# Kernel optimization log

Measured on AMD Instinct MI355X. Metric: run time of the kernel, lower is better.

The kernel has to match this reference:

```python
import jax, jax.numpy as jnp
import numpy as np

D_MODEL = 1024
N_HEADS = 16
D_HEAD = D_MODEL // N_HEADS


def setup_inputs() -> dict:
    key = jax.random.key(0)
    ks = jax.random.split(key, 5)
    B, T = 2, 2048
    x = jax.random.normal(ks[0], (B, T, D_MODEL), dtype=jnp.float32)
    s = 1.0 / np.sqrt(D_MODEL)
    W_qkv = jax.random.normal(ks[1], (D_MODEL, 3 * D_MODEL), dtype=jnp.float32) * s
    b_qkv = jnp.zeros((3 * D_MODEL,), dtype=jnp.float32)
    W_proj = jax.random.normal(ks[2], (D_MODEL, D_MODEL), dtype=jnp.float32) * s
    b_proj = jnp.zeros((D_MODEL,), dtype=jnp.float32)
    return {"x": x, "W_qkv": W_qkv, "b_qkv": b_qkv, "W_proj": W_proj, "b_proj": b_proj}


def reference(x, W_qkv, b_qkv, W_proj, b_proj):
    B, T, C = x.shape
    qkv = x @ W_qkv + b_qkv                      # [B,T,3C]
    q, k, v = jnp.split(qkv, 3, axis=-1)
    # [B,T,C] -> [B,H,T,Dh]
    def to_heads(t):
        return t.reshape(B, T, N_HEADS, D_HEAD).transpose(0, 2, 1, 3)
    q, k, v = to_heads(q), to_heads(k), to_heads(v)
    scale = 1.0 / np.sqrt(D_HEAD).astype(np.float32)
    scores = jnp.einsum('bhqd,bhkd->bhqk', q, k) * scale  # [B,H,T,T]
    causal = jnp.tril(jnp.ones((T, T), dtype=bool))
    scores = jnp.where(causal, scores, -jnp.inf)
    attn = jax.nn.softmax(scores, axis=-1)
    out = jnp.einsum('bhqk,bhkd->bhqd', attn, v)          # [B,H,T,Dh]
    out = out.transpose(0, 2, 1, 3).reshape(B, T, C)
    return out @ W_proj + b_proj
```

## Files before the change

### kernel.cpp

```cpp
#include <hip/hip_runtime.h>
#include <hip/hip_bf16.h>
#include <cstdint>


using u16 = unsigned short;
using u32 = unsigned int;

typedef __bf16 bf16x8 __attribute__((ext_vector_type(8)));
typedef float f32x4 __attribute__((ext_vector_type(4)));

#define AS1 __attribute__((address_space(1)))
#define AS3 __attribute__((address_space(3)))

__device__ __forceinline__ u16 f2bf(float f) {
  u32 u = __float_as_uint(f);
  u += 0x7fffu + ((u >> 16) & 1u);
  return (u16)(u >> 16);
}
__device__ __forceinline__ u32 pack2bf(float a, float b) {
  u32 ua = __float_as_uint(a) + 0x8000u;
  u32 ub = __float_as_uint(b) + 0x8000u;
  return (ua >> 16) | (ub & 0xffff0000u);
}

__global__ __launch_bounds__(256) void prep(const float* __restrict__ x,
                                            u16* __restrict__ xb,
                                            const float* __restrict__ W0,
                                            u16* __restrict__ T0,
                                            const float* __restrict__ W1,
                                            u16* __restrict__ T1) {
  const int bx = blockIdx.x;
  const int tid = threadIdx.x;
  if (bx < 4096) {
    const int i = bx * 256 + tid;
    float4 v = ((const float4*)x)[i];
    ushort4 o;
    o.x = f2bf(v.x); o.y = f2bf(v.y); o.z = f2bf(v.z); o.w = f2bf(v.w);
    ((ushort4*)xb)[i] = o;
    return;
  }
  __shared__ float t[32][33];
  const int idx = bx - 4096;
  const int bxx = idx & 127, by = idx >> 7;
  const float* W; u16* Wt; int N, n0;
  if (bxx < 96) { W = W0; Wt = T0; N = 3072; n0 = bxx * 32; }
  else          { W = W1; Wt = T1; N = 1024; n0 = (bxx - 96) * 32; }
  const int k0 = by * 32;
  const int tx = tid & 31, ty = tid >> 5;
#pragma unroll
  for (int i = 0; i < 4; ++i)
    t[ty + i * 8][tx] = W[(size_t)(k0 + ty + i * 8) * N + n0 + tx];
  __syncthreads();
#pragma unroll
  for (int i = 0; i < 4; ++i)
    Wt[(size_t)(n0 + ty + i * 8) * 1024 + k0 + tx] = f2bf(t[tx][ty + i * 8]);
}

__global__ __launch_bounds__(256) void gemm_qkv(const u16* __restrict__ A,
                                                const u16* __restrict__ Bt,
                                                const float* __restrict__ bias,
                                                u16* __restrict__ qb,
                                                u16* __restrict__ KF,
                                                u16* __restrict__ VF,
                                                float sc_val) {
  constexpr int BM = 128, BK = 32;
  constexpr int K = 1024;
  __shared__ __align__(16) u16 lA[BM * BK];
  __shared__ __align__(16) u16 lB[BM * BK];
  const int tid  = threadIdx.x;
  const int lane = tid & 63;
  const int wave = tid >> 6;
  const int bm = blockIdx.x * BM;
  const int bn = blockIdx.y * BM;
  const int wr = (wave >> 1) * 64;
  const int wc = (wave & 1) * 64;

  f32x4 acc[4][4] = {};

  const int f0 = (wave << 10) + (lane << 4);
  const int f1 = f0 + 4096;
  const int r0 = f0 >> 6, c0 = (f0 & 63) >> 1;
  const int r1 = f1 >> 6, c1 = (f1 & 63) >> 1;

  const int arow = wr + (lane & 15);
  const int brow = wc + (lane & 15);
  const int kk   = (lane >> 4) << 3;

  for (int k0 = 0; k0 < K; k0 += BK) {
    __builtin_amdgcn_global_load_lds((AS1 const void*)(A + (size_t)(bm + r0) * K + k0 + c0),
                                     (AS3 void*)(lA + (wave << 9)), 16, 0, 0);
    __builtin_amdgcn_global_load_lds((AS1 const void*)(A + (size_t)(bm + r1) * K + k0 + c1),
                                     (AS3 void*)(lA + ((wave + 4) << 9)), 16, 0, 0);
    __builtin_amdgcn_global_load_lds((AS1 const void*)(Bt + (size_t)(bn + r0) * K + k0 + c0),
                                     (AS3 void*)(lB + (wave << 9)), 16, 0, 0);
    __builtin_amdgcn_global_load_lds((AS1 const void*)(Bt + (size_t)(bn + r1) * K + k0 + c1),
                                     (AS3 void*)(lB + ((wave + 4) << 9)), 16, 0, 0);
    __syncthreads();

    bf16x8 af[4], bfr[4];
#pragma unroll
    for (int mi = 0; mi < 4; ++mi)
      af[mi] = *(const bf16x8*)&lA[(arow + mi * 16) * BK + kk];
#pragma unroll
    for (int ni = 0; ni < 4; ++ni)
      bfr[ni] = *(const bf16x8*)&lB[(brow + ni * 16) * BK + kk];
#pragma unroll
    for (int mi = 0; mi < 4; ++mi)
#pragma unroll
      for (int ni = 0; ni < 4; ++ni)
        acc[mi][ni] = __builtin_amdgcn_mfma_f32_16x16x32_bf16(af[mi], bfr[ni],
                                                              acc[mi][ni], 0, 0, 0);
    __syncthreads();
  }

  const int crow0 = bm + wr + ((lane >> 4) << 2);
  const int ccol0 = bn + wc + (lane & 15);
  if (bn < 1024) {
#pragma unroll
    for (int ni = 0; ni < 4; ++ni) {
      const int n = ccol0 + ni * 16;
      const float bv = bias[n];
#pragma unroll
      for (int mi = 0; mi < 4; ++mi) {
        const int m0 = crow0 + mi * 16;
#pragma unroll
        for (int r = 0; r < 4; ++r)
          qb[(size_t)(m0 + r) * 1024 + n] = f2bf((acc[mi][ni][r] + bv) * sc_val);
      }
    }
  } else if (bn < 2048) {
#pragma unroll
    for (int ni = 0; ni < 4; ++ni) {
      const int n  = ccol0 + ni * 16;
      const int hk = (n - 1024) >> 6;
      const int d  = (n - 1024) & 63;
      const int hh = d >> 5, qd = (d >> 3) & 3, j = d & 7;
      const float bv = bias[n];
#pragma unroll
      for (int mi = 0; mi < 4; ++mi) {
#pragma unroll
        for (int r = 0; r < 4; ++r) {
          const int t  = crow0 + mi * 16 + r;
          const int bb = t >> 11, tt = t & 2047;
          const int kt = tt >> 6, mm = (tt >> 4) & 3, l = tt & 15;
          KF[((size_t)((bb * 16 + hk) * 32 + kt) * 8 + mm * 2 + hh) * 512 +
             (qd * 16 + l) * 8 + j] = f2bf(acc[mi][ni][r] + bv);
        }
      }
    }
  } else {
#pragma unroll
    for (int ni = 0; ni < 4; ++ni) {
      const int n  = ccol0 + ni * 16;
      const int hv = (n - 2048) >> 6;
      const int d  = (n - 2048) & 63;
      const int di = d >> 4, l = d & 15;
      const float bv = bias[n];
#pragma unroll
      for (int mi = 0; mi < 4; ++mi) {
#pragma unroll
        for (int r = 0; r < 4; ++r) {
          const int t  = crow0 + mi * 16 + r;
          const int bb = t >> 11, tt = t & 2047;
          const int kt = tt >> 6, to = tt & 63;
          const int mq = to >> 4, qd2 = (to >> 2) & 3, rr = to & 3;
          const int hh = mq >> 1, j = (mq & 1) * 4 + rr;
          VF[((size_t)((bb * 16 + hv) * 32 + kt) * 8 + hh * 4 + di) * 512 +
             (qd2 * 16 + l) * 8 + j] = f2bf(acc[mi][ni][r] + bv);
        }
      }
    }
  }
}

__global__ __launch_bounds__(256) void gemm_proj(const u16* __restrict__ A,
                                                 const u16* __restrict__ Bt,
                                                 const float* __restrict__ bias,
                                                 float* __restrict__ C) {
  constexpr int BM = 128, BN = 64, BK = 32;
  constexpr int K = 1024, N = 1024;
  __shared__ __align__(16) u16 lA[BM * BK];
  __shared__ __align__(16) u16 lB[BN * BK];
  const int tid  = threadIdx.x;
  const int lane = tid & 63;
  const int wave = tid >> 6;
  const int bm = blockIdx.x * BM;
  const int bn = blockIdx.y * BN;
  const int wr = wave * 32;

  f32x4 acc[2][4] = {};

  const int f0 = (wave << 10) + (lane << 4);
  const int f1 = f0 + 4096;
  const int ar0 = f0 >> 6, ac0 = (f0 & 63) >> 1;
  const int ar1 = f1 >> 6, ac1 = (f1 & 63) >> 1;

  const int arow = wr + (lane & 15);
  const int brow = (lane & 15);
  const int kk   = (lane >> 4) << 3;

  for (int k0 = 0; k0 < K; k0 += BK) {
    __builtin_amdgcn_global_load_lds((AS1 const void*)(A + (size_t)(bm + ar0) * K + k0 + ac0),
                                     (AS3 void*)(lA + (wave << 9)), 16, 0, 0);
    __builtin_amdgcn_global_load_lds((AS1 const void*)(A + (size_t)(bm + ar1) * K + k0 + ac1),
                                     (AS3 void*)(lA + ((wave + 4) << 9)), 16, 0, 0);
    __builtin_amdgcn_global_load_lds((AS1 const void*)(Bt + (size_t)(bn + ar0) * K + k0 + ac0),
                                     (AS3 void*)(lB + (wave << 9)), 16, 0, 0);
    __syncthreads();

    bf16x8 af[2], bfr[4];
#pragma unroll
    for (int mi = 0; mi < 2; ++mi)
      af[mi] = *(const bf16x8*)&lA[(arow + mi * 16) * BK + kk];
#pragma unroll
    for (int ni = 0; ni < 4; ++ni)
      bfr[ni] = *(const bf16x8*)&lB[(brow + ni * 16) * BK + kk];
#pragma unroll
    for (int mi = 0; mi < 2; ++mi)
#pragma unroll
      for (int ni = 0; ni < 4; ++ni)
        acc[mi][ni] = __builtin_amdgcn_mfma_f32_16x16x32_bf16(af[mi], bfr[ni],
                                                              acc[mi][ni], 0, 0, 0);
    __syncthreads();
  }

  const int crow0 = bm + wr + ((lane >> 4) << 2);
  const int ccol0 = bn + (lane & 15);
#pragma unroll
  for (int ni = 0; ni < 4; ++ni) {
    const int n = ccol0 + ni * 16;
    const float bv = bias[n];
#pragma unroll
    for (int mi = 0; mi < 2; ++mi) {
      const int m0 = crow0 + mi * 16;
#pragma unroll
      for (int r = 0; r < 4; ++r)
        C[(size_t)(m0 + r) * N + n] = acc[mi][ni][r] + bv;
    }
  }
}

__global__ __launch_bounds__(256) void attn_bal(const u16* __restrict__ qb,
                                                const u16* __restrict__ KF,
                                                const u16* __restrict__ VF,
                                                u16* __restrict__ out) {
  const int u  = blockIdx.x;
  const int bh = blockIdx.y;
  const int b = bh >> 4, h = bh & 15;
  const int tid = threadIdx.x;
  const int lane = tid & 63;
  const int w    = tid >> 6;
  const int quad = lane >> 4;
  const int l15  = lane & 15;
  const int g32 = (w & 1) ? (63 - u) : u;
  const int par = w >> 1;
  const int q0 = g32 * 32;
  const int ktmax = g32 >> 1;

  __shared__ float CB[2][64][35];

  const u16* qbase = qb + (size_t)b * 2048 * 1024 + h * 64;
  bf16x8 qf[2][2];
#pragma unroll
  for (int g = 0; g < 2; ++g)
#pragma unroll
    for (int hh = 0; hh < 2; ++hh)
      qf[g][hh] = *(const bf16x8*)(qbase + (size_t)(q0 + g * 16 + l15) * 1024 +
                                   hh * 32 + quad * 8);

  const size_t fb = (size_t)bh * 32 * 4096 + lane * 8;
  const u16* kfb = KF + fb;
  const u16* vfb = VF + fb;

  f32x4 accO[2][4] = {};
  float lrow[2] = {0.f, 0.f};

  bf16x8 kcur[4][2];
  {
    const u16* kp = kfb + (size_t)par * 4096;
#pragma unroll
    for (int m = 0; m < 4; ++m)
#pragma unroll
      for (int hh = 0; hh < 2; ++hh)
        kcur[m][hh] = *(const bf16x8*)(kp + (m * 2 + hh) * 512);
  }

  for (int kt = par; kt <= ktmax; kt += 2) {
    const u16* vp = vfb + (size_t)kt * 4096;
    bf16x8 vfr[2][4];
#pragma unroll
    for (int hh = 0; hh < 2; ++hh)
#pragma unroll
      for (int di = 0; di < 4; ++di)
        vfr[hh][di] = *(const bf16x8*)(vp + (hh * 4 + di) * 512);
    const int ktn = (kt + 2 <= ktmax) ? kt + 2 : ktmax;
    const u16* kpn = kfb + (size_t)ktn * 4096;
    bf16x8 knx[4][2];
#pragma unroll
    for (int m = 0; m < 4; ++m)
#pragma unroll
      for (int hh = 0; hh < 2; ++hh)
        knx[m][hh] = *(const bf16x8*)(kpn + (m * 2 + hh) * 512);

    const bool diag = (kt == ktmax);
    bf16x8 ap[2][2];
#pragma unroll
    for (int g = 0; g < 2; ++g) {
      f32x4 sT[4] = {};
#pragma unroll
      for (int m = 0; m < 4; ++m) {
        sT[m] = __builtin_amdgcn_mfma_f32_16x16x32_bf16(kcur[m][0], qf[g][0], sT[m], 0, 0, 0);
        sT[m] = __builtin_amdgcn_mfma_f32_16x16x32_bf16(kcur[m][1], qf[g][1], sT[m], 0, 0, 0);
      }
      float pv[4][4];
      if (diag) {
        const int qgl = q0 + g * 16 + l15;
#pragma unroll
        for (int m = 0; m < 4; ++m)
#pragma unroll
          for (int r = 0; r < 4; ++r) {
            const bool msk = (kt * 64 + m * 16 + quad * 4 + r) > qgl;
            pv[m][r] = msk ? 0.f : __builtin_amdgcn_exp2f(sT[m][r]);
          }
      } else {
#pragma unroll
        for (int m = 0; m < 4; ++m)
#pragma unroll
          for (int r = 0; r < 4; ++r)
            pv[m][r] = __builtin_amdgcn_exp2f(sT[m][r]);
      }
      const float s0 = (pv[0][0] + pv[0][1]) + (pv[0][2] + pv[0][3]);
      const float s1 = (pv[1][0] + pv[1][1]) + (pv[1][2] + pv[1][3]);
      const float s2 = (pv[2][0] + pv[2][1]) + (pv[2][2] + pv[2][3]);
      const float s3 = (pv[3][0] + pv[3][1]) + (pv[3][2] + pv[3][3]);
      lrow[g] += (s0 + s1) + (s2 + s3);

      union { u32 u4[4]; bf16x8 v; } t0, t1;
      t0.u4[0] = pack2bf(pv[0][0], pv[0][1]);
      t0.u4[1] = pack2bf(pv[0][2], pv[0][3]);
      t0.u4[2] = pack2bf(pv[1][0], pv[1][1]);
      t0.u4[3] = pack2bf(pv[1][2], pv[1][3]);
      t1.u4[0] = pack2bf(pv[2][0], pv[2][1]);
      t1.u4[1] = pack2bf(pv[2][2], pv[2][3]);
      t1.u4[2] = pack2bf(pv[3][0], pv[3][1]);
      t1.u4[3] = pack2bf(pv[3][2], pv[3][3]);
      ap[g][0] = t0.v;
      ap[g][1] = t1.v;
    }

#pragma unroll
    for (int hh = 0; hh < 2; ++hh)
#pragma unroll
      for (int di = 0; di < 4; ++di) {
        bf16x8 bv = vfr[hh][di];
#pragma unroll
        for (int g = 0; g < 2; ++g)
          accO[g][di] = __builtin_amdgcn_mfma_f32_16x16x32_bf16(ap[g][hh], bv,
                                                               accO[g][di], 0, 0, 0);
      }

#pragma unroll
    for (int m = 0; m < 4; ++m)
#pragma unroll
      for (int hh = 0; hh < 2; ++hh)
        kcur[m][hh] = knx[m][hh];
  }

  if (par) {
    float* cb = CB[w & 1][lane];
#pragma unroll
    for (int g = 0; g < 2; ++g)
#pragma unroll
      for (int di = 0; di < 4; ++di)
#pragma unroll
        for (int r = 0; r < 4; ++r)
          cb[g * 16 + di * 4 + r] = accO[g][di][r];
    cb[32] = lrow[0];
    cb[33] = lrow[1];
  }
  __syncthreads();
  if (!par) {
    const float* cb = CB[w & 1][lane];
#pragma unroll
    for (int g = 0; g < 2; ++g)
#pragma unroll
      for (int di = 0; di < 4; ++di)
#pragma unroll
        for (int r = 0; r < 4; ++r)
          accO[g][di][r] += cb[g * 16 + di * 4 + r];
    lrow[0] += cb[32];
    lrow[1] += cb[33];
#pragma unroll
    for (int g = 0; g < 2; ++g) {
      lrow[g] += __shfl_xor(lrow[g], 16);
      lrow[g] += __shfl_xor(lrow[g], 32);
    }

#pragma unroll
    for (int g = 0; g < 2; ++g)
#pragma unroll
      for (int r = 0; r < 4; ++r) {
        const float lv = __shfl(lrow[g], quad * 4 + r);
        const float inv = 1.f / lv;
        const int q = q0 + g * 16 + quad * 4 + r;
        u16* op = out + (size_t)(b * 2048 + q) * 1024 + h * 64 + l15;
#pragma unroll
        for (int di = 0; di < 4; ++di)
          op[di * 16] = f2bf(accO[g][di][r] * inv);
      }
  }
}

extern "C" void kernel_launch(void* const* d_in, const int* in_sizes, int n_in,
                              void* d_out, int out_size, void* d_ws, size_t ws_size,
                              hipStream_t stream) {
  const float* x     = (const float*)d_in[0];
  const float* Wqkv  = (const float*)d_in[1];
  const float* bqkv  = (const float*)d_in[2];
  const float* Wproj = (const float*)d_in[3];
  const float* bproj = (const float*)d_in[4];
  float* out = (float*)d_out;

  char* ws = (char*)d_ws;
  u16* xb     = (u16*)(ws);
  u16* wqkvT  = (u16*)(ws + 8388608);
  u16* wprojT = (u16*)(ws + 14680064);
  u16* qb     = (u16*)(ws + 16777216);
  u16* KF     = (u16*)(ws + 25165824);
  u16* VF     = (u16*)(ws + 33554432);
  u16* att    = (u16*)(ws + 41943040);

  constexpr float cs = 0.18033688011f;

  prep<<<8192, 256, 0, stream>>>(x, xb, Wqkv, wqkvT, Wproj, wprojT);

  gemm_qkv<<<dim3(32, 24), 256, 0, stream>>>(xb, wqkvT, bqkv, qb, KF, VF, cs);

  attn_bal<<<dim3(32, 32), 256, 0, stream>>>(qb, KF, VF, att);

  gemm_proj<<<dim3(32, 16), 256, 0, stream>>>(att, wprojT, bproj, out);
}
```

Measured before the change: 185.6 us.

## Rewrite QKV GEMM as 256x256 double-buffered pipelined kernel with swizzled LDS

The QKV projection GEMM moves from 128x128 tiles with a single LDS buffer and two full barriers per 32-wide k-step to 256x256 tiles with 512 threads. It now uses BK=64, double-buffered LDS, and XOR-swizzled LDS addressing to avoid bank conflicts. Global-to-LDS loads for the next tiles are interleaved between four MFMA phases, with s_setprio raised around the MFMA work. Block IDs are remapped by XCD so blocks that share A and B tiles land on the same die's L2. The aim is to hide load latency and raise MFMA utilisation, at the cost of 128KB of LDS, high register pressure, and only 192 blocks, which may underfill the CUs.

Result: faster. 176.6 us (-4.8%).

```diff
diff --git a/kernel.cpp b/kernel.cpp
--- a/kernel.cpp
+++ b/kernel.cpp
@@ -56,72 +56,166 @@
     Wt[(size_t)(n0 + ty + i * 8) * 1024 + k0 + tx] = f2bf(t[tx][ty + i * 8]);
 }
 
-__global__ __launch_bounds__(256) void gemm_qkv(const u16* __restrict__ A,
-                                                const u16* __restrict__ Bt,
-                                                const float* __restrict__ bias,
-                                                u16* __restrict__ qb,
-                                                u16* __restrict__ KF,
-                                                u16* __restrict__ VF,
-                                                float sc_val) {
-  constexpr int BM = 128, BK = 32;
-  constexpr int K = 1024;
-  __shared__ __align__(16) u16 lA[BM * BK];
-  __shared__ __align__(16) u16 lB[BM * BK];
+#define MFMA16 __builtin_amdgcn_mfma_f32_16x16x32_bf16
+
+__global__ __launch_bounds__(512, 2) void gemm_qkv(const u16* __restrict__ A,
+                                                   const u16* __restrict__ Bt,
+                                                   const float* __restrict__ bias,
+                                                   u16* __restrict__ qb,
+                                                   u16* __restrict__ KF,
+                                                   u16* __restrict__ VF,
+                                                   float sc_val) {
+  constexpr int NT = 16;
+  __shared__ __align__(16) u16 sm[2 * 4 * 8192];
+
   const int tid  = threadIdx.x;
   const int lane = tid & 63;
-  const int wave = tid >> 6;
-  const int bm = blockIdx.x * BM;
-  const int bn = blockIdx.y * BM;
-  const int wr = (wave >> 1) * 64;
-  const int wc = (wave & 1) * 64;
-
-  f32x4 acc[4][4] = {};
-
-  const int f0 = (wave << 10) + (lane << 4);
-  const int f1 = f0 + 4096;
-  const int r0 = f0 >> 6, c0 = (f0 & 63) >> 1;
-  const int r1 = f1 >> 6, c1 = (f1 & 63) >> 1;
-
-  const int arow = wr + (lane & 15);
-  const int brow = wc + (lane & 15);
-  const int kk   = (lane >> 4) << 3;
-
-  for (int k0 = 0; k0 < K; k0 += BK) {
-    __builtin_amdgcn_global_load_lds((AS1 const void*)(A + (size_t)(bm + r0) * K + k0 + c0),
-                                     (AS3 void*)(lA + (wave << 9)), 16, 0, 0);
-    __builtin_amdgcn_global_load_lds((AS1 const void*)(A + (size_t)(bm + r1) * K + k0 + c1),
-                                     (AS3 void*)(lA + ((wave + 4) << 9)), 16, 0, 0);
-    __builtin_amdgcn_global_load_lds((AS1 const void*)(Bt + (size_t)(bn + r0) * K + k0 + c0),
-                                     (AS3 void*)(lB + (wave << 9)), 16, 0, 0);
-    __builtin_amdgcn_global_load_lds((AS1 const void*)(Bt + (size_t)(bn + r1) * K + k0 + c1),
-                                     (AS3 void*)(lB + ((wave + 4) << 9)), 16, 0, 0);
-    __syncthreads();
-
-    bf16x8 af[4], bfr[4];
+  const int w    = tid >> 6;
+  const int quad = lane >> 4;
+  const int l15  = lane & 15;
+
+  const int bid = blockIdx.x;
+  const int xcd = bid & 7, c = bid >> 3;
+  const int mt = (xcd >> 1) * 4 + (c & 3);
+  const int nt = (xcd & 1) * 6 + (c >> 2);
+  const int bm = mt * 256, bn = nt * 256;
+
+  const int wr = (w >> 2) * 128;
+  const int wc = (w & 3) * 64;
+
+  const int rowS = w * 8 + (lane >> 3);
+  const int scol = (((lane & 7) ^ (lane >> 3)) << 3);
+
+#define STAGE(matp, rowbase, ldsoff, ktile)                                     \
+  do {                                                                          \
+    const u16* _s = (matp) + ((size_t)((rowbase) + rowS) << 10) +               \
+                    ((ktile) << 6) + scol;                                      \
+    u16* _d = sm + (ldsoff) + (w << 9);                                         \
+    __builtin_amdgcn_global_load_lds((AS1 const void*)_s, (AS3 void*)_d,        \
+                                     16, 0, 0);                                 \
+    __builtin_amdgcn_global_load_lds((AS1 const void*)(_s + (64 << 10)),        \
+                                     (AS3 void*)(_d + 4096), 16, 0, 0);         \
+  } while (0)
+
+  const int raoff = (wr >> 7) * 8192;
+  const int rboff = (2 + (wc >> 7)) * 8192;
+  const int av0 = l15 * 64 + ((quad ^ (l15 & 7)) << 3);
+  const int av1 = l15 * 64 + (((4 + quad) ^ (l15 & 7)) << 3);
+  const int bv0 = ((wc & 64) + l15) * 64 + ((quad ^ (l15 & 7)) << 3);
+  const int bv1 = ((wc & 64) + l15) * 64 + (((4 + quad) ^ (l15 & 7)) << 3);
+
+  STAGE(A,  bm,       0 * 8192, 0);
+  STAGE(A,  bm + 128, 1 * 8192, 0);
+  STAGE(Bt, bn,       2 * 8192, 0);
+  STAGE(Bt, bn + 128, 3 * 8192, 0);
+  STAGE(Bt, bn,       32768 + 2 * 8192, 1);
+  STAGE(A,  bm,       32768 + 0 * 8192, 1);
+  STAGE(A,  bm + 128, 32768 + 1 * 8192, 1);
+  asm volatile("s_waitcnt vmcnt(6)" ::: "memory");
+  __builtin_amdgcn_s_barrier();
+
+  f32x4 acc[8][4] = {};
+  bf16x8 a[4][2], b[4][2];
+
+#pragma unroll 2
+  for (int kt = 0; kt < NT; ++kt) {
+    const int bo  = (kt & 1) * 32768;
+    const int nbo = bo ^ 32768;
+    const u16* smA = sm + bo + raoff;
+    const u16* smB = sm + bo + rboff;
+
+#pragma unroll
+    for (int mi = 0; mi < 4; ++mi) {
+      a[mi][0] = *(const bf16x8*)(smA + mi * 1024 + av0);
+      a[mi][1] = *(const bf16x8*)(smA + mi * 1024 + av1);
+    }
+#pragma unroll
+    for (int ni = 0; ni < 2; ++ni) {
+      b[ni][0] = *(const bf16x8*)(smB + ni * 1024 + bv0);
+      b[ni][1] = *(const bf16x8*)(smB + ni * 1024 + bv1);
+    }
+    if (kt + 1 < NT) STAGE(Bt, bn + 128, nbo + 3 * 8192, kt + 1);
+    __builtin_amdgcn_s_barrier();
+    asm volatile("s_waitcnt lgkmcnt(0)" ::: "memory");
+    __builtin_amdgcn_s_setprio(1);
 #pragma unroll
     for (int mi = 0; mi < 4; ++mi)
-      af[mi] = *(const bf16x8*)&lA[(arow + mi * 16) * BK + kk];
-#pragma unroll
-    for (int ni = 0; ni < 4; ++ni)
-      bfr[ni] = *(const bf16x8*)&lB[(brow + ni * 16) * BK + kk];
+#pragma unroll
+      for (int ni = 0; ni < 2; ++ni) {
+        acc[mi][ni] = MFMA16(a[mi][0], b[ni][0], acc[mi][ni], 0, 0, 0);
+        acc[mi][ni] = MFMA16(a[mi][1], b[ni][1], acc[mi][ni], 0, 0, 0);
+      }
+    __builtin_amdgcn_s_setprio(0);
+    __builtin_amdgcn_s_barrier();
+
+#pragma unroll
+    for (int ni = 2; ni < 4; ++ni) {
+      b[ni][0] = *(const bf16x8*)(smB + ni * 1024 + bv0);
+      b[ni][1] = *(const bf16x8*)(smB + ni * 1024 + bv1);
+    }
+    __builtin_amdgcn_s_barrier();
+    asm volatile("s_waitcnt lgkmcnt(0)" ::: "memory");
+    __builtin_amdgcn_s_setprio(1);
 #pragma unroll
     for (int mi = 0; mi < 4; ++mi)
 #pragma unroll
-      for (int ni = 0; ni < 4; ++ni)
-        acc[mi][ni] = __builtin_amdgcn_mfma_f32_16x16x32_bf16(af[mi], bfr[ni],
-                                                              acc[mi][ni], 0, 0, 0);
-    __syncthreads();
-  }
-
-  const int crow0 = bm + wr + ((lane >> 4) << 2);
-  const int ccol0 = bn + wc + (lane & 15);
+      for (int ni = 2; ni < 4; ++ni) {
+        acc[mi][ni] = MFMA16(a[mi][0], b[ni][0], acc[mi][ni], 0, 0, 0);
+        acc[mi][ni] = MFMA16(a[mi][1], b[ni][1], acc[mi][ni], 0, 0, 0);
+      }
+    __builtin_amdgcn_s_setprio(0);
+    __builtin_amdgcn_s_barrier();
+
+#pragma unroll
+    for (int mi = 0; mi < 4; ++mi) {
+      a[mi][0] = *(const bf16x8*)(smA + (4 + mi) * 1024 + av0);
+      a[mi][1] = *(const bf16x8*)(smA + (4 + mi) * 1024 + av1);
+    }
+    if (kt + 2 < NT) STAGE(Bt, bn, bo + 2 * 8192, kt + 2);
+    __builtin_amdgcn_s_barrier();
+    asm volatile("s_waitcnt lgkmcnt(0)" ::: "memory");
+    __builtin_amdgcn_s_setprio(1);
+#pragma unroll
+    for (int mi = 0; mi < 4; ++mi)
+#pragma unroll
+      for (int ni = 2; ni < 4; ++ni) {
+        acc[4 + mi][ni] = MFMA16(a[mi][0], b[ni][0], acc[4 + mi][ni], 0, 0, 0);
+        acc[4 + mi][ni] = MFMA16(a[mi][1], b[ni][1], acc[4 + mi][ni], 0, 0, 0);
+      }
+    __builtin_amdgcn_s_setprio(0);
+    __builtin_amdgcn_s_barrier();
+
+    if (kt + 2 < NT) {
+      STAGE(A, bm,       bo + 0 * 8192, kt + 2);
+      STAGE(A, bm + 128, bo + 1 * 8192, kt + 2);
+    }
+    __builtin_amdgcn_s_barrier();
+    __builtin_amdgcn_s_setprio(1);
+#pragma unroll
+    for (int mi = 0; mi < 4; ++mi)
+#pragma unroll
+      for (int ni = 0; ni < 2; ++ni) {
+        acc[4 + mi][ni] = MFMA16(a[mi][0], b[ni][0], acc[4 + mi][ni], 0, 0, 0);
+        acc[4 + mi][ni] = MFMA16(a[mi][1], b[ni][1], acc[4 + mi][ni], 0, 0, 0);
+      }
+    __builtin_amdgcn_s_setprio(0);
+    if (kt + 2 < NT)
+      asm volatile("s_waitcnt vmcnt(6)" ::: "memory");
+    else
+      asm volatile("s_waitcnt vmcnt(0)" ::: "memory");
+    __builtin_amdgcn_s_barrier();
+  }
+#undef STAGE
+
+  const int crow0 = bm + wr + (quad << 2);
+  const int ccol0 = bn + wc + l15;
   if (bn < 1024) {
 #pragma unroll
     for (int ni = 0; ni < 4; ++ni) {
       const int n = ccol0 + ni * 16;
       const float bv = bias[n];
 #pragma unroll
-      for (int mi = 0; mi < 4; ++mi) {
+      for (int mi = 0; mi < 8; ++mi) {
         const int m0 = crow0 + mi * 16;
 #pragma unroll
         for (int r = 0; r < 4; ++r)
@@ -137,7 +231,7 @@
       const int hh = d >> 5, qd = (d >> 3) & 3, j = d & 7;
       const float bv = bias[n];
 #pragma unroll
-      for (int mi = 0; mi < 4; ++mi) {
+      for (int mi = 0; mi < 8; ++mi) {
 #pragma unroll
         for (int r = 0; r < 4; ++r) {
           const int t  = crow0 + mi * 16 + r;
@@ -157,7 +251,7 @@
       const int di = d >> 4, l = d & 15;
       const float bv = bias[n];
 #pragma unroll
-      for (int mi = 0; mi < 4; ++mi) {
+      for (int mi = 0; mi < 8; ++mi) {
 #pragma unroll
         for (int r = 0; r < 4; ++r) {
           const int t  = crow0 + mi * 16 + r;
@@ -434,7 +528,7 @@
 
   prep<<<8192, 256, 0, stream>>>(x, xb, Wqkv, wqkvT, Wproj, wprojT);
 
-  gemm_qkv<<<dim3(32, 24), 256, 0, stream>>>(xb, wqkvT, bqkv, qb, KF, VF, cs);
+  gemm_qkv<<<dim3(192), 512, 0, stream>>>(xb, wqkvT, bqkv, qb, KF, VF, cs);
 
   attn_bal<<<dim3(32, 32), 256, 0, stream>>>(qb, KF, VF, att);
 
```
